# Kernel tuning notes

Hardware: AMD Instinct MI355X
Metric: run time of the kernel (lower is better)

Reference implementation:

```python
import jax, jax.numpy as jnp
import numpy as np

N = 1200          # number of mentions in the block -> NxN SDP matrix
HID = 128         # MLP hidden width
RANK = 64         # Burer-Monteiro factor rank ~ sqrt(2N)
SDP_ITERS = 100   # fixed iteration budget (original caps at 50000)
BN_EPS = 1e-5


def setup_inputs() -> dict:
    key = jax.random.key(0)
    k = jax.random.split(key, 5)
    P = N * (N - 1) // 2
    x = jax.random.normal(k[0], (P, 39), jnp.float32)
    W1 = jax.random.normal(k[1], (39, HID), jnp.float32) * (1.0 / np.sqrt(39.0))
    b1 = jnp.zeros((HID,), jnp.float32)
    gamma = jnp.ones((HID,), jnp.float32)
    beta = jnp.zeros((HID,), jnp.float32)
    W2 = jax.random.normal(k[2], (HID, 1), jnp.float32) * (1.0 / np.sqrt(float(HID)))
    b2 = jnp.zeros((1,), jnp.float32)
    V0 = jax.random.normal(k[3], (N, RANK), jnp.float32)
    return {"x": x, "W1": W1, "b1": b1, "gamma": gamma, "beta": beta,
            "W2": W2, "b2": b2, "V0": V0}


def _forward(x, W1, b1, gamma, beta, W2, b2, V0):
    # MLPLayer: Linear -> BatchNorm (batch stats) -> ReLU -> Linear(->1)
    h = x @ W1 + b1                                   # [P, HID]
    mu = h.mean(axis=0)
    var = h.var(axis=0)
    h = (h - mu) * jax.lax.rsqrt(var + BN_EPS) * gamma + beta
    h = jax.nn.relu(h)
    w = (h @ W2 + b2).reshape(-1)                     # flat edge weights [P]

    # UncompressTransformLayer: flat upper-triangle -> symmetric NxN, zero diag
    iu, ju = jnp.triu_indices(N, k=1)
    A = jnp.zeros((N, N), w.dtype).at[iu, ju].set(w)
    W = A + A.T                                       # [N, N]

    # SDPLayer: max <W, X> s.t. X PSD, diag(X)=1, X>=0 via Burer-Monteiro
    # low-rank factorization with fixed-iteration projected gradient ascent.
    V = V0 / jnp.linalg.norm(V0, axis=1, keepdims=True)
    lr = 1.0 / (jnp.linalg.norm(W) + 1e-8)

    def step(V, _):
        V = V + lr * (W @ V)
        V = V / jnp.linalg.norm(V, axis=1, keepdims=True)
        return V, None

    V, _ = jax.lax.scan(step, V, None, length=SDP_ITERS)
    X = jnp.clip(V @ V.T, 0.0, 1.0)                   # output probabilities [N, N]
    return X


def reference(x, W1, b1, gamma, beta, W2, b2, V0):
    return _forward(x, W1, b1, gamma, beta, W2, b2, V0)
```

## Files before the change

kernel.cpp:

```cpp
#include <hip/hip_runtime.h>

#define NM 1200
#define PP 719400
#define HID 128
#define RANK 64
#define SDP_ITERS 100

#define OFF_S      0
#define OFF_SUMW2  1600
#define OFF_CVEC   1664
#define OFF_W1S    1792
#define OFF_WVEC   6912
#define OFF_WMAT   726400
#define OFF_VA     2166400
#define OFF_VB     2243200

__device__ __forceinline__ float wave_reduce_sum(float v) {
#pragma unroll
    for (int o = 32; o > 0; o >>= 1) v += __shfl_xor(v, o, 64);
    return v;
}

__global__ __launch_bounds__(256) void zero_kernel(float* __restrict__ ws, int n) {
    int i = blockIdx.x * 256 + threadIdx.x;
    if (i < n) ws[i] = 0.0f;
}

#define STATS_BLOCKS 1024
#define KT 40
__global__ __launch_bounds__(256) void stats_kernel(const float* __restrict__ x,
                                                    float* __restrict__ S) {
    __shared__ __align__(8) float tile[KT * 48];
    __shared__ float Sacc[48 * 48];
    const int tid = threadIdx.x;
    for (int i = tid; i < 48 * 48; i += 256) Sacc[i] = 0.f;

    const int rpb = (PP + STATS_BLOCKS - 1) / STATS_BLOCKS;
    const int r0 = blockIdx.x * rpb;
    const int r1 = min(r0 + rpb, PP);

    const int z  = tid >> 6;
    const int ln = tid & 63;
    const int ty = ln >> 3, tx = ln & 7;

    float acc[6][6];
#pragma unroll
    for (int a = 0; a < 6; ++a)
#pragma unroll
        for (int b = 0; b < 6; ++b) acc[a][b] = 0.f;

    for (int t = r0; t < r1; t += KT) {
        const int nr = min(KT, r1 - t);
        __syncthreads();
        const float* xg = x + (size_t)t * 39;
        for (int idx = tid; idx < KT * 48; idx += 256) {
            int rr = idx / 48, cc = idx - rr * 48;
            float v = 0.f;
            if (rr < nr) {
                if (cc < 39) v = xg[rr * 39 + cc];
                else if (cc == 39) v = 1.0f;
            }
            tile[idx] = v;
        }
        __syncthreads();
#pragma unroll 2
        for (int kk = 0; kk < KT / 4; ++kk) {
            const float* row = &tile[(kk * 4 + z) * 48];
            float2 a0 = *(const float2*)(row + ty * 6);
            float2 a1 = *(const float2*)(row + ty * 6 + 2);
            float2 a2 = *(const float2*)(row + ty * 6 + 4);
            float2 b0 = *(const float2*)(row + tx * 6);
            float2 b1 = *(const float2*)(row + tx * 6 + 2);
            float2 b2 = *(const float2*)(row + tx * 6 + 4);
            float av[6] = {a0.x, a0.y, a1.x, a1.y, a2.x, a2.y};
            float bv[6] = {b0.x, b0.y, b1.x, b1.y, b2.x, b2.y};
#pragma unroll
            for (int a = 0; a < 6; ++a)
#pragma unroll
                for (int b = 0; b < 6; ++b)
                    acc[a][b] = fmaf(av[a], bv[b], acc[a][b]);
        }
    }
    __syncthreads();
#pragma unroll
    for (int a = 0; a < 6; ++a)
#pragma unroll
        for (int b = 0; b < 6; ++b)
            atomicAdd(&Sacc[(ty * 6 + a) * 48 + tx * 6 + b], acc[a][b]);
    __syncthreads();
    for (int i = tid; i < 1600; i += 256) {
        int r = i / 40, c = i - r * 40;
        atomicAdd(&S[i], Sacc[r * 48 + c]);
    }
}

__global__ __launch_bounds__(64) void bn_prep(const float* __restrict__ S,
                                              const float* __restrict__ W1,
                                              const float* __restrict__ gamma,
                                              const float* __restrict__ beta,
                                              float* __restrict__ W1s,
                                              float* __restrict__ cvec) {
    const int j = blockIdx.x;
    const int l = threadIdx.x;
    const float invP = 1.0f / (float)PP;
    float q = 0.f;
    for (int idx = l; idx < 39 * 39; idx += 64) {
        int a = idx / 39, b = idx - a * 39;
        q = fmaf(S[a * 40 + b], W1[a * HID + j] * W1[b * HID + j], q);
    }
    float s1 = (l < 39) ? (S[39 * 40 + l] * invP) * W1[l * HID + j] : 0.f;
    q = wave_reduce_sum(q);
    s1 = wave_reduce_sum(s1);
    float var = q * invP - s1 * s1;
    float scale = gamma[j] * (1.0f / sqrtf(var + 1e-5f));
    for (int a = l; a < 39; a += 64) W1s[a * HID + j] = W1[a * HID + j] * scale;
    if (l == 0) cvec[j] = -s1 * scale + beta[j];
}

__global__ __launch_bounds__(256) void mlp_kernel(const float* __restrict__ x,
                                                  const float* __restrict__ W1s,
                                                  const float* __restrict__ cvec,
                                                  const float* __restrict__ W2,
                                                  const float* __restrict__ b2,
                                                  float* __restrict__ w,
                                                  float* __restrict__ sumw2) {
    __shared__ float xt[256 * 39];
    __shared__ float red[4];
    const size_t base = (size_t)blockIdx.x * 256;
    {
        const size_t g0 = base * 39;
        const size_t gmax = (size_t)PP * 39;
        for (int idx = threadIdx.x; idx < 256 * 39; idx += 256) {
            size_t g = g0 + idx;
            xt[idx] = (g < gmax) ? x[g] : 0.f;
        }
    }
    __syncthreads();

    float xr[39];
    {
        const float* xrow = &xt[threadIdx.x * 39];
#pragma unroll
        for (int k = 0; k < 39; ++k) xr[k] = xrow[k];
    }

    float wacc = 0.f;
#pragma unroll 1
    for (int c = 0; c < 2; ++c) {
        float acc[64];
#pragma unroll
        for (int jj = 0; jj < 64; ++jj) acc[jj] = cvec[c * 64 + jj];
#pragma unroll 3
        for (int k = 0; k < 39; ++k) {
            const float xk = xr[k];
            const float* wrow = &W1s[k * HID + c * 64];
#pragma unroll
            for (int jj = 0; jj < 64; ++jj) acc[jj] = fmaf(xk, wrow[jj], acc[jj]);
        }
#pragma unroll
        for (int jj = 0; jj < 64; ++jj)
            wacc = fmaf(fmaxf(acc[jj], 0.f), W2[c * 64 + jj], wacc);
    }

    const size_t p = base + threadIdx.x;
    const float wv = wacc + b2[0];
    float sq = 0.f;
    if (p < (size_t)PP) { w[p] = wv; sq = wv * wv; }
    sq = wave_reduce_sum(sq);
    if ((threadIdx.x & 63) == 0) red[threadIdx.x >> 6] = sq;
    __syncthreads();
    if (threadIdx.x == 0) atomicAdd(sumw2, red[0] + red[1] + red[2] + red[3]);
}

__global__ __launch_bounds__(256) void buildW(const float* __restrict__ w,
                                              float* __restrict__ W) {
    __shared__ float tile[16][17];
    const int bi = blockIdx.y, bj = blockIdx.x;
    if (bi > bj) return;
    const int ty = threadIdx.x >> 4, tx = threadIdx.x & 15;
    const int i = bi * 16 + ty, j = bj * 16 + tx;
    float v = 0.f;
    if (i < j) {
        int p = i * (NM - 1) - (i * (i - 1)) / 2 + (j - i - 1);
        v = w[p];
    }
    tile[ty][tx] = v;
    __syncthreads();
    if (bi == bj) {
        float out = (i < j) ? v : ((i > j) ? tile[tx][ty] : 0.f);
        W[(size_t)i * NM + j] = out;
    } else {
        W[(size_t)i * NM + j] = v;
        W[(size_t)(bj * 16 + ty) * NM + (bi * 16 + tx)] = tile[tx][ty];
    }
}

__global__ __launch_bounds__(256) void v0norm(const float* __restrict__ V0,
                                              float* __restrict__ V) {
    const int i = blockIdx.x * 4 + (threadIdx.x >> 6);
    const int c = threadIdx.x & 63;
    float v = V0[(size_t)i * RANK + c];
    float s = wave_reduce_sum(v * v);
    V[(size_t)i * RANK + c] = v * (1.0f / sqrtf(s));
}

__global__ __launch_bounds__(512) void sdp_step(const float* __restrict__ Vin,
                                                float* __restrict__ Vout,
                                                const float* __restrict__ W,
                                                const float* __restrict__ sumw2) {
    __shared__ float part[8][6][64];
    const int tid = threadIdx.x;
    const int c = tid & 63;
    const int wvid = tid >> 6;
    const int i0 = blockIdx.x * 6;
    const int j0 = __builtin_amdgcn_readfirstlane(wvid * 150);

    const float* __restrict__ Wb = W + (size_t)i0 * NM + j0;
    const float* __restrict__ Vb = Vin + (size_t)j0 * RANK + c;

    float acc[6] = {0.f, 0.f, 0.f, 0.f, 0.f, 0.f};
#pragma unroll 10
    for (int t = 0; t < 150; ++t) {
        const float vc = Vb[(size_t)t * RANK];
#pragma unroll
        for (int r = 0; r < 6; ++r)
            acc[r] = fmaf(Wb[(size_t)r * NM + t], vc, acc[r]);
    }
#pragma unroll
    for (int r = 0; r < 6; ++r) part[wvid][r][c] = acc[r];
    __syncthreads();

    if (tid < 384) {
        const int r2 = tid >> 6, c2 = tid & 63;
        float s = 0.f;
#pragma unroll
        for (int k = 0; k < 8; ++k) s += part[k][r2][c2];
        const float lr = 1.0f / (sqrtf(2.0f * sumw2[0]) + 1e-8f);
        float y = Vin[(size_t)(i0 + r2) * RANK + c2] + lr * s;
        float n = wave_reduce_sum(y * y);
        Vout[(size_t)(i0 + r2) * RANK + c2] = y * (1.0f / sqrtf(n));
    }
}

__global__ __launch_bounds__(256) void vvt_kernel(const float* __restrict__ V,
                                                  float* __restrict__ out) {
    const int bi = blockIdx.y, bj = blockIdx.x;
    if (bi > bj) return;
    __shared__ __align__(16) float Ti[64][132];
    __shared__ __align__(16) float Tj[64][132];
    const int tid = threadIdx.x;
    for (int idx = tid; idx < 128 * 64; idx += 256) {
        int row = idx >> 6, k = idx & 63;
        int gi = bi * 128 + row, gj = bj * 128 + row;
        Ti[k][row] = (gi < NM) ? V[(size_t)gi * RANK + k] : 0.f;
        Tj[k][row] = (gj < NM) ? V[(size_t)gj * RANK + k] : 0.f;
    }
    __syncthreads();
    const int ty = tid >> 4, tx = tid & 15;
    float acc[8][8];
#pragma unroll
    for (int a = 0; a < 8; ++a)
#pragma unroll
        for (int b = 0; b < 8; ++b) acc[a][b] = 0.f;
    for (int k = 0; k < 64; ++k) {
        float4 a0 = *(const float4*)&Ti[k][ty * 8];
        float4 a1 = *(const float4*)&Ti[k][ty * 8 + 4];
        float4 b0 = *(const float4*)&Tj[k][tx * 8];
        float4 b1 = *(const float4*)&Tj[k][tx * 8 + 4];
        float av[8] = {a0.x, a0.y, a0.z, a0.w, a1.x, a1.y, a1.z, a1.w};
        float bv[8] = {b0.x, b0.y, b0.z, b0.w, b1.x, b1.y, b1.z, b1.w};
#pragma unroll
        for (int a = 0; a < 8; ++a)
#pragma unroll
            for (int b = 0; b < 8; ++b)
                acc[a][b] = fmaf(av[a], bv[b], acc[a][b]);
    }
#pragma unroll
    for (int a = 0; a < 8; ++a) {
        int i = bi * 128 + 8 * ty + a;
        if (i >= NM) break;
        int jb = bj * 128 + 8 * tx;
        if (jb + 7 < NM) {
            float4 s0 = {fminf(fmaxf(acc[a][0], 0.f), 1.f), fminf(fmaxf(acc[a][1], 0.f), 1.f),
                         fminf(fmaxf(acc[a][2], 0.f), 1.f), fminf(fmaxf(acc[a][3], 0.f), 1.f)};
            float4 s1 = {fminf(fmaxf(acc[a][4], 0.f), 1.f), fminf(fmaxf(acc[a][5], 0.f), 1.f),
                         fminf(fmaxf(acc[a][6], 0.f), 1.f), fminf(fmaxf(acc[a][7], 0.f), 1.f)};
            *(float4*)&out[(size_t)i * NM + jb] = s0;
            *(float4*)&out[(size_t)i * NM + jb + 4] = s1;
        } else {
#pragma unroll
            for (int b = 0; b < 8; ++b) {
                int j = jb + b;
                if (j < NM) out[(size_t)i * NM + j] = fminf(fmaxf(acc[a][b], 0.f), 1.f);
            }
        }
    }
    if (bi != bj) {
#pragma unroll
        for (int b = 0; b < 8; ++b) {
            int j = bj * 128 + 8 * tx + b;
            if (j >= NM) break;
            int ib = bi * 128 + 8 * ty;
            if (ib + 7 < NM) {
                float4 s0 = {fminf(fmaxf(acc[0][b], 0.f), 1.f), fminf(fmaxf(acc[1][b], 0.f), 1.f),
                             fminf(fmaxf(acc[2][b], 0.f), 1.f), fminf(fmaxf(acc[3][b], 0.f), 1.f)};
                float4 s1 = {fminf(fmaxf(acc[4][b], 0.f), 1.f), fminf(fmaxf(acc[5][b], 0.f), 1.f),
                             fminf(fmaxf(acc[6][b], 0.f), 1.f), fminf(fmaxf(acc[7][b], 0.f), 1.f)};
                *(float4*)&out[(size_t)j * NM + ib] = s0;
                *(float4*)&out[(size_t)j * NM + ib + 4] = s1;
            } else {
#pragma unroll
                for (int a = 0; a < 8; ++a) {
                    int i = ib + a;
                    if (i < NM) out[(size_t)j * NM + i] = fminf(fmaxf(acc[a][b], 0.f), 1.f);
                }
            }
        }
    }
}

extern "C" void kernel_launch(void* const* d_in, const int* in_sizes, int n_in,
                              void* d_out, int out_size, void* d_ws, size_t ws_size,
                              hipStream_t stream) {
    const float* x     = (const float*)d_in[0];
    const float* W1    = (const float*)d_in[1];
    const float* gamma = (const float*)d_in[3];
    const float* beta  = (const float*)d_in[4];
    const float* W2    = (const float*)d_in[5];
    const float* b2    = (const float*)d_in[6];
    const float* V0    = (const float*)d_in[7];
    float* out = (float*)d_out;

    float* ws    = (float*)d_ws;
    float* S     = ws + OFF_S;
    float* sumw2 = ws + OFF_SUMW2;
    float* cvec  = ws + OFF_CVEC;
    float* W1s   = ws + OFF_W1S;
    float* wvec  = ws + OFF_WVEC;
    float* Wmat  = ws + OFF_WMAT;
    float* Va    = ws + OFF_VA;
    float* Vb    = ws + OFF_VB;

    zero_kernel<<<7, 256, 0, stream>>>(ws, OFF_W1S);
    stats_kernel<<<STATS_BLOCKS, 256, 0, stream>>>(x, S);
    bn_prep<<<HID, 64, 0, stream>>>(S, W1, gamma, beta, W1s, cvec);
    mlp_kernel<<<(PP + 255) / 256, 256, 0, stream>>>(x, W1s, cvec, W2, b2, wvec, sumw2);
    buildW<<<dim3(75, 75), 256, 0, stream>>>(wvec, Wmat);
    v0norm<<<NM / 4, 256, 0, stream>>>(V0, Va);
    for (int it = 0; it < SDP_ITERS; ++it) {
        const float* vin = (it & 1) ? Vb : Va;
        float* vout      = (it & 1) ? Va : Vb;
        sdp_step<<<NM / 6, 512, 0, stream>>>(vin, vout, Wmat, sumw2);
    }
    vvt_kernel<<<dim3(10, 10), 256, 0, stream>>>(Va, out);
}
```

Measured before the change: 1.341 ms.

## Fuse SDP iterations into persistent kernel with grid barrier; double-buffer stats tiles

Replaces the 100 separate sdp_step launches with a single persistent kernel of 240 blocks, each handling 5 rows. Blocks synchronize between iterations through a global atomic counter and generation barrier, which removes per-iteration launch overhead. The stats kernel also double-buffers its shared tile and prefetches the next chunk into registers with vectorized stores, so loads overlap with the FMA loop. The grid barrier assumes all 240 blocks are co-resident, and the barrier words sit in the zeroed workspace region, which must be cleared before each run.

After: 2.970 ms. +121.4%, slower.

```diff
diff --git a/kernel.cpp b/kernel.cpp
--- a/kernel.cpp
+++ b/kernel.cpp
@@ -8,6 +8,7 @@
 
 #define OFF_S      0
 #define OFF_SUMW2  1600
+#define OFF_BAR    1632
 #define OFF_CVEC   1664
 #define OFF_W1S    1792
 #define OFF_WVEC   6912
@@ -30,15 +31,29 @@
 #define KT 40
 __global__ __launch_bounds__(256) void stats_kernel(const float* __restrict__ x,
                                                     float* __restrict__ S) {
-    __shared__ __align__(8) float tile[KT * 48];
+    __shared__ __align__(16) float tile[2][KT * 48];
     __shared__ float Sacc[48 * 48];
     const int tid = threadIdx.x;
     for (int i = tid; i < 48 * 48; i += 256) Sacc[i] = 0.f;
+    for (int i = tid; i < 2 * KT * 8; i += 256) {
+        int b = i / (KT * 8);
+        int rem = i - b * (KT * 8);
+        int r = rem >> 3, k = rem & 7;
+        tile[b][r * 48 + 40 + k] = 0.f;
+    }
 
     const int rpb = (PP + STATS_BLOCKS - 1) / STATS_BLOCKS;
     const int r0 = blockIdx.x * rpb;
     const int r1 = min(r0 + rpb, PP);
 
+    const bool stg = tid < 200;
+    const int sr = tid / 5;
+    const int sc = (tid - sr * 5) * 8;
+    float* const dA = &tile[0][sr * 48 + sc];
+    float* const dB = &tile[1][sr * 48 + sc];
+    const float* const srcb = x + (size_t)sr * 39 + sc;
+    const bool tail = (sc == 32);
+
     const int z  = tid >> 6;
     const int ln = tid & 63;
     const int ty = ln >> 3, tx = ln & 7;
@@ -49,23 +64,44 @@
 #pragma unroll
         for (int b = 0; b < 6; ++b) acc[a][b] = 0.f;
 
+    float v[8];
+    {
+        const float* s = srcb + (size_t)r0 * 39;
+        const bool ok = stg && (r0 + sr < r1);
+#pragma unroll
+        for (int k = 0; k < 8; ++k) v[k] = 0.f;
+        if (ok) {
+#pragma unroll
+            for (int k = 0; k < 7; ++k) v[k] = s[k];
+            v[7] = tail ? 1.0f : s[7];
+        }
+    }
+    if (stg) {
+        *(float4*)dA       = make_float4(v[0], v[1], v[2], v[3]);
+        *(float4*)(dA + 4) = make_float4(v[4], v[5], v[6], v[7]);
+    }
+    __syncthreads();
+
+    int cur = 0;
     for (int t = r0; t < r1; t += KT) {
-        const int nr = min(KT, r1 - t);
-        __syncthreads();
-        const float* xg = x + (size_t)t * 39;
-        for (int idx = tid; idx < KT * 48; idx += 256) {
-            int rr = idx / 48, cc = idx - rr * 48;
-            float v = 0.f;
-            if (rr < nr) {
-                if (cc < 39) v = xg[rr * 39 + cc];
-                else if (cc == 39) v = 1.0f;
+        const int tn = t + KT;
+        const bool more = tn < r1;
+        float vn[8];
+        if (more) {
+            const float* s = srcb + (size_t)tn * 39;
+            const bool ok = stg && (tn + sr < r1);
+#pragma unroll
+            for (int k = 0; k < 8; ++k) vn[k] = 0.f;
+            if (ok) {
+#pragma unroll
+                for (int k = 0; k < 7; ++k) vn[k] = s[k];
+                vn[7] = tail ? 1.0f : s[7];
             }
-            tile[idx] = v;
-        }
-        __syncthreads();
+        }
+        const float* tb = tile[cur];
 #pragma unroll 2
         for (int kk = 0; kk < KT / 4; ++kk) {
-            const float* row = &tile[(kk * 4 + z) * 48];
+            const float* row = &tb[(kk * 4 + z) * 48];
             float2 a0 = *(const float2*)(row + ty * 6);
             float2 a1 = *(const float2*)(row + ty * 6 + 2);
             float2 a2 = *(const float2*)(row + ty * 6 + 4);
@@ -80,8 +116,15 @@
                 for (int b = 0; b < 6; ++b)
                     acc[a][b] = fmaf(av[a], bv[b], acc[a][b]);
         }
-    }
-    __syncthreads();
+        if (more && stg) {
+            float* d = cur ? dA : dB;
+            *(float4*)d       = make_float4(vn[0], vn[1], vn[2], vn[3]);
+            *(float4*)(d + 4) = make_float4(vn[4], vn[5], vn[6], vn[7]);
+        }
+        __syncthreads();
+        cur ^= 1;
+    }
+
 #pragma unroll
     for (int a = 0; a < 6; ++a)
 #pragma unroll
@@ -204,41 +247,64 @@
     V[(size_t)i * RANK + c] = v * (1.0f / sqrtf(s));
 }
 
-__global__ __launch_bounds__(512) void sdp_step(const float* __restrict__ Vin,
-                                                float* __restrict__ Vout,
-                                                const float* __restrict__ W,
-                                                const float* __restrict__ sumw2) {
-    __shared__ float part[8][6][64];
+#define SDP_BLOCKS 240
+#define ROWS_PB 5
+__global__ __launch_bounds__(512) void sdp_persist(float* __restrict__ Va,
+                                                   float* __restrict__ Vb,
+                                                   const float* __restrict__ W,
+                                                   const float* __restrict__ sumw2,
+                                                   int* bar) {
+    __shared__ float part[8][ROWS_PB][64];
     const int tid = threadIdx.x;
     const int c = tid & 63;
     const int wvid = tid >> 6;
-    const int i0 = blockIdx.x * 6;
+    const int i0 = blockIdx.x * ROWS_PB;
     const int j0 = __builtin_amdgcn_readfirstlane(wvid * 150);
-
+    const float lr = 1.0f / (sqrtf(2.0f * sumw2[0]) + 1e-8f);
     const float* __restrict__ Wb = W + (size_t)i0 * NM + j0;
-    const float* __restrict__ Vb = Vin + (size_t)j0 * RANK + c;
-
-    float acc[6] = {0.f, 0.f, 0.f, 0.f, 0.f, 0.f};
+
+    for (int it = 0; it < SDP_ITERS; ++it) {
+        const float* __restrict__ Vin = (it & 1) ? Vb : Va;
+        float* __restrict__ Vout      = (it & 1) ? Va : Vb;
+        const float* __restrict__ Vbase = Vin + (size_t)j0 * RANK + c;
+
+        float acc[ROWS_PB] = {0.f, 0.f, 0.f, 0.f, 0.f};
 #pragma unroll 10
-    for (int t = 0; t < 150; ++t) {
-        const float vc = Vb[(size_t)t * RANK];
-#pragma unroll
-        for (int r = 0; r < 6; ++r)
-            acc[r] = fmaf(Wb[(size_t)r * NM + t], vc, acc[r]);
-    }
-#pragma unroll
-    for (int r = 0; r < 6; ++r) part[wvid][r][c] = acc[r];
-    __syncthreads();
-
-    if (tid < 384) {
-        const int r2 = tid >> 6, c2 = tid & 63;
-        float s = 0.f;
-#pragma unroll
-        for (int k = 0; k < 8; ++k) s += part[k][r2][c2];
-        const float lr = 1.0f / (sqrtf(2.0f * sumw2[0]) + 1e-8f);
-        float y = Vin[(size_t)(i0 + r2) * RANK + c2] + lr * s;
-        float n = wave_reduce_sum(y * y);
-        Vout[(size_t)(i0 + r2) * RANK + c2] = y * (1.0f / sqrtf(n));
+        for (int t = 0; t < 150; ++t) {
+            const float vc = Vbase[(size_t)t * RANK];
+#pragma unroll
+            for (int r = 0; r < ROWS_PB; ++r)
+                acc[r] = fmaf(Wb[(size_t)r * NM + t], vc, acc[r]);
+        }
+#pragma unroll
+        for (int r = 0; r < ROWS_PB; ++r) part[wvid][r][c] = acc[r];
+        __syncthreads();
+
+        if (tid < ROWS_PB * 64) {
+            const int r2 = tid >> 6, c2 = tid & 63;
+            float s = 0.f;
+#pragma unroll
+            for (int k = 0; k < 8; ++k) s += part[k][r2][c2];
+            float y = Vin[(size_t)(i0 + r2) * RANK + c2] + lr * s;
+            float n = wave_reduce_sum(y * y);
+            Vout[(size_t)(i0 + r2) * RANK + c2] = y * (1.0f / sqrtf(n));
+        }
+
+        __syncthreads();
+        if (tid == 0) {
+            __threadfence();
+            if (__hip_atomic_fetch_add(&bar[0], 1, __ATOMIC_ACQ_REL,
+                                       __HIP_MEMORY_SCOPE_AGENT) == SDP_BLOCKS - 1) {
+                __hip_atomic_store(&bar[0], 0, __ATOMIC_RELAXED, __HIP_MEMORY_SCOPE_AGENT);
+                __hip_atomic_store(&bar[1], it + 1, __ATOMIC_RELEASE, __HIP_MEMORY_SCOPE_AGENT);
+            } else {
+                while (__hip_atomic_load(&bar[1], __ATOMIC_ACQUIRE,
+                                         __HIP_MEMORY_SCOPE_AGENT) <= it) {
+                    __builtin_amdgcn_s_sleep(1);
+                }
+            }
+        }
+        __syncthreads();
     }
 }
 
@@ -347,10 +413,6 @@
     mlp_kernel<<<(PP + 255) / 256, 256, 0, stream>>>(x, W1s, cvec, W2, b2, wvec, sumw2);
     buildW<<<dim3(75, 75), 256, 0, stream>>>(wvec, Wmat);
     v0norm<<<NM / 4, 256, 0, stream>>>(V0, Va);
-    for (int it = 0; it < SDP_ITERS; ++it) {
-        const float* vin = (it & 1) ? Vb : Va;
-        float* vout      = (it & 1) ? Va : Vb;
-        sdp_step<<<NM / 6, 512, 0, stream>>>(vin, vout, Wmat, sumw2);
-    }
+    sdp_persist<<<SDP_BLOCKS, 512, 0, stream>>>(Va, Vb, Wmat, sumw2, (int*)(ws + OFF_BAR));
     vvt_kernel<<<dim3(10, 10), 256, 0, stream>>>(Va, out);
 }
```
